# Kernel optimization log

Measured on AMD Instinct MI355X. Metric: run time of the kernel, lower is better.

Reference implementation:

```python
import jax, jax.numpy as jnp
import numpy as np

N = 100000
F_IN = 128
H = 128
E = 1600000
EP = 200000


def _gcn_conv(x, W, b, src, dst, n):
    # GCNConv (PyG default): add self-loops done by caller; symmetric norm; linear + scatter-add.
    xw = x @ W                                        # [n, H]
    deg = jax.ops.segment_sum(jnp.ones(src.shape[0], x.dtype), dst, num_segments=n)
    dinv = jnp.where(deg > 0, jax.lax.rsqrt(deg), 0.0)
    norm = dinv[src] * dinv[dst]                      # [E']
    msg = xw[src] * norm[:, None]                     # [E', H] gather
    out = jax.ops.segment_sum(msg, dst, num_segments=n)  # scatter-add
    return out + b


def setup_inputs() -> dict:
    key = jax.random.key(0)
    k = jax.random.split(key, 9)
    x = jax.random.normal(k[0], (N, F_IN), dtype=jnp.float32)
    edge_index = jax.random.randint(k[1], (2, E), 0, N, dtype=jnp.int64)
    dict_node = jax.random.randint(k[2], (N,), 0, N, dtype=jnp.int64)
    pos_edge_index = jax.random.randint(k[3], (2, EP), 0, N, dtype=jnp.int64)
    neg_edge_index = jax.random.randint(k[4], (2, EP), 0, N, dtype=jnp.int64)
    s1 = 1.0 / np.sqrt(F_IN)
    s2 = 1.0 / np.sqrt(H)
    W1 = jax.random.uniform(k[5], (F_IN, H), jnp.float32, -s1, s1)
    b1 = jnp.zeros((H,), jnp.float32)
    W2 = jax.random.uniform(k[6], (H, H), jnp.float32, -s2, s2)
    b2 = jnp.zeros((H,), jnp.float32)
    return {"x": x, "W1": W1, "b1": b1, "W2": W2, "b2": b2,
            "edge_index": edge_index, "dict_node": dict_node,
            "pos_edge_index": pos_edge_index, "neg_edge_index": neg_edge_index}


def reference(x, W1, b1, W2, b2, edge_index, dict_node, pos_edge_index, neg_edge_index):
    n = x.shape[0]
    # add self-loops once (both convs use the same edge_index)
    loop = jnp.arange(n, dtype=edge_index.dtype)
    src = jnp.concatenate([edge_index[0], loop])
    dst = jnp.concatenate([edge_index[1], loop])
    # encode (dropout p=0.01 is identity in eval mode)
    h = jax.nn.relu(_gcn_conv(x, W1, b1, src, dst, n))
    h = jax.nn.relu(_gcn_conv(h, W2, b2, src, dst, n))
    # global_mean_pool over dict_node segments (size = num_nodes)
    sums = jax.ops.segment_sum(h, dict_node, num_segments=n)
    cnt = jax.ops.segment_sum(jnp.ones((n,), h.dtype), dict_node, num_segments=n)
    z = sums / jnp.maximum(cnt, 1.0)[:, None]
    # decode: per-edge dot products over concatenated pos/neg edges
    ei = jnp.concatenate([pos_edge_index, neg_edge_index], axis=-1)
    logits = jnp.sum(z[ei[0]] * z[ei[1]], axis=-1)
    return logits
```

## Files before the change

kernel.cpp:

```cpp
#include <hip/hip_runtime.h>
#include <hip/hip_fp16.h>

#define HH 128
#define SCAN_T 256
#define SCAN_C 2048
#define PCHUNK 16384


__global__ void hist_k(const int* __restrict__ key, int* __restrict__ hist, int e) {
  int i = blockIdx.x * blockDim.x + threadIdx.x;
  if (i < e) atomicAdd(&hist[key[i]], 1);
}

__global__ __launch_bounds__(SCAN_T) void scan_pass1_k(const int* __restrict__ hist,
                                                       int* __restrict__ bsum, int n) {
  __shared__ int lds[SCAN_T];
  int base = blockIdx.x * SCAN_C + threadIdx.x * 8;
  int s = 0;
  #pragma unroll
  for (int k = 0; k < 8; ++k) { int i = base + k; if (i < n) s += hist[i]; }
  lds[threadIdx.x] = s;
  __syncthreads();
  for (int off = 128; off > 0; off >>= 1) {
    if (threadIdx.x < off) lds[threadIdx.x] += lds[threadIdx.x + off];
    __syncthreads();
  }
  if (threadIdx.x == 0) bsum[blockIdx.x] = lds[0];
}

__global__ __launch_bounds__(SCAN_T) void scan_pass2_k(int* __restrict__ bsum, int nb,
                                                       int* __restrict__ rowptr_n, int total) {
  __shared__ int lds[SCAN_T];
  int v = (threadIdx.x < nb) ? bsum[threadIdx.x] : 0;
  lds[threadIdx.x] = v;
  __syncthreads();
  for (int off = 1; off < SCAN_T; off <<= 1) {
    int t = (threadIdx.x >= off) ? lds[threadIdx.x - off] : 0;
    __syncthreads();
    lds[threadIdx.x] += t;
    __syncthreads();
  }
  if (threadIdx.x < nb) bsum[threadIdx.x] = (threadIdx.x == 0) ? 0 : lds[threadIdx.x - 1];
  if (threadIdx.x == 0) *rowptr_n = total;
}

__global__ __launch_bounds__(SCAN_T) void scan_pass3_k(int* __restrict__ tmp,
                                                       const int* __restrict__ bsum,
                                                       int* __restrict__ rowptr,
                                                       float* __restrict__ dinv, int n) {
  __shared__ int lds[SCAN_T];
  int base = blockIdx.x * SCAN_C + threadIdx.x * 8;
  int v[8]; int s = 0;
  #pragma unroll
  for (int k = 0; k < 8; ++k) { int i = base + k; v[k] = (i < n) ? tmp[i] : 0; s += v[k]; }
  lds[threadIdx.x] = s;
  __syncthreads();
  for (int off = 1; off < SCAN_T; off <<= 1) {
    int t = (threadIdx.x >= off) ? lds[threadIdx.x - off] : 0;
    __syncthreads();
    lds[threadIdx.x] += t;
    __syncthreads();
  }
  int run = bsum[blockIdx.x] + ((threadIdx.x == 0) ? 0 : lds[threadIdx.x - 1]);
  #pragma unroll
  for (int k = 0; k < 8; ++k) {
    int i = base + k;
    if (i < n) {
      rowptr[i] = run;
      tmp[i] = run;
      if (dinv) dinv[i] = rsqrtf((float)v[k] + 1.0f);
      run += v[k];
    }
  }
}

__global__ void build_nodes_k(const int* __restrict__ dict, int* __restrict__ cursor,
                              int* __restrict__ nodelist, int n) {
  int i = blockIdx.x * blockDim.x + threadIdx.x;
  if (i < n) {
    int pos = atomicAdd(&cursor[dict[i]], 1);
    nodelist[pos] = i;
  }
}


__global__ __launch_bounds__(256) void part_count_k(const int* __restrict__ dst, int e,
                                                    int nbkt, int nblk,
                                                    int* __restrict__ gcnt,
                                                    int* __restrict__ blkoff) {
  __shared__ int h[512];
  for (int i = threadIdx.x; i < nbkt; i += 256) h[i] = 0;
  __syncthreads();
  int start = blockIdx.x * PCHUNK;
  int cnt = e - start; if (cnt > PCHUNK) cnt = PCHUNK;
  for (int i = threadIdx.x; i < cnt; i += 256)
    atomicAdd(&h[dst[start + i] >> 8], 1);
  __syncthreads();
  for (int i = threadIdx.x; i < nbkt; i += 256) {
    int c = h[i];
    if (c) blkoff[(size_t)i * nblk + blockIdx.x] = atomicAdd(&gcnt[i], c);
  }
}

__global__ __launch_bounds__(512) void scan_bkt_k(const int* __restrict__ gcnt,
                                                  int* __restrict__ bktbase, int nbkt, int e) {
  __shared__ int sc[512];
  int tid = threadIdx.x;
  int v = (tid < nbkt) ? gcnt[tid] : 0;
  sc[tid] = v;
  __syncthreads();
  for (int off = 1; off < 512; off <<= 1) {
    int t = (tid >= off) ? sc[tid - off] : 0;
    __syncthreads();
    sc[tid] += t;
    __syncthreads();
  }
  if (tid < nbkt) bktbase[tid] = sc[tid] - v;
  if (tid == 0) bktbase[nbkt] = e;
}

__global__ __launch_bounds__(256) void part_scatter_k(const int* __restrict__ src,
                                                      const int* __restrict__ dst, int e,
                                                      int nbkt, int nblk,
                                                      const int* __restrict__ bktbase,
                                                      const int* __restrict__ blkoff,
                                                      int2* __restrict__ part) {
  __shared__ int cur[512];
  for (int i = threadIdx.x; i < nbkt; i += 256)
    cur[i] = bktbase[i] + blkoff[(size_t)i * nblk + blockIdx.x];
  __syncthreads();
  int start = blockIdx.x * PCHUNK;
  int cnt = e - start; if (cnt > PCHUNK) cnt = PCHUNK;
  for (int i = threadIdx.x; i < cnt; i += 256) {
    int d = dst[start + i], s = src[start + i];
    int pos = atomicAdd(&cur[d >> 8], 1);
    part[pos] = make_int2(s, d);
  }
}

__global__ __launch_bounds__(256) void bucket_csr_k(const int2* __restrict__ part,
                                                    const int* __restrict__ bktbase,
                                                    int* __restrict__ rowptr,
                                                    float* __restrict__ dinv,
                                                    int* __restrict__ esrc,
                                                    int n, int e, int nbkt) {
  __shared__ int hist[256];
  __shared__ int sc[256];
  __shared__ int cur[256];
  int tid = threadIdx.x;
  int b = blockIdx.x;
  int dstbase = b << 8;
  int nloc = n - dstbase; if (nloc > 256) nloc = 256;
  int beg = bktbase[b], bend = bktbase[b + 1];

  hist[tid] = 0;
  __syncthreads();
  for (int j = beg + tid; j < bend; j += 256)
    atomicAdd(&hist[part[j].y & 255], 1);
  __syncthreads();
  int v = hist[tid];
  sc[tid] = v;
  __syncthreads();
  for (int off = 1; off < 256; off <<= 1) {
    int t = (tid >= off) ? sc[tid - off] : 0;
    __syncthreads();
    sc[tid] += t;
    __syncthreads();
  }
  int excl = sc[tid] - v;
  if (tid < nloc) {
    rowptr[dstbase + tid] = beg + excl;
    cur[tid] = beg + excl;
    dinv[dstbase + tid] = rsqrtf((float)v + 1.0f);
  }
  __syncthreads();
  for (int j = beg + tid; j < bend; j += 256) {
    int2 p = part[j];
    int pos = atomicAdd(&cur[p.y & 255], 1);
    esrc[pos] = p.x;
  }
  if (b == nbkt - 1 && tid == 0) rowptr[n] = e;
}

template <bool OUT16>
__global__ __launch_bounds__(256) void gemm128_v3(const float* __restrict__ A,
                                                  const float* __restrict__ W,
                                                  const float* __restrict__ dscale,
                                                  void* __restrict__ out, int n) {
  __shared__ float As[64][129];
  const int tid = threadIdx.x;
  const int rbase = blockIdx.x * 64;

  const int vrows = (n - rbase) < 64 ? (n - rbase) : 64;
  const int maxf4 = vrows * 32;
  const float4* Ag = (const float4*)(A + (size_t)rbase * HH);
  #pragma unroll
  for (int j = 0; j < 8; ++j) {
    int f = tid + 256 * j;
    int r = f >> 5, c4 = f & 31;
    float4 v = (f < maxf4) ? Ag[f] : make_float4(0.f, 0.f, 0.f, 0.f);
    As[r][c4 * 4 + 0] = v.x;
    As[r][c4 * 4 + 1] = v.y;
    As[r][c4 * 4 + 2] = v.z;
    As[r][c4 * 4 + 3] = v.w;
  }
  __syncthreads();

  const int r = tid & 63;
  const int q = __builtin_amdgcn_readfirstlane(tid >> 6);
  const float* Asr = &As[r][0];
  const float* Wq = W + q * 32;

  float4 acc[8];
  #pragma unroll
  for (int c = 0; c < 8; ++c) acc[c] = make_float4(0.f, 0.f, 0.f, 0.f);

  #pragma unroll 4
  for (int k = 0; k < HH; ++k) {
    float a = Asr[k];
    const float4* Wr = (const float4*)(Wq + (size_t)k * HH);
    #pragma unroll
    for (int c = 0; c < 8; ++c) {
      float4 w = Wr[c];
      acc[c].x += a * w.x; acc[c].y += a * w.y;
      acc[c].z += a * w.z; acc[c].w += a * w.w;
    }
  }

  int row = rbase + r;
  if (row < n) {
    float s = dscale ? dscale[row] : 1.0f;
    if (OUT16) {
      uint2* o = (uint2*)((__half*)out + (size_t)row * HH) + q * 8;
      #pragma unroll
      for (int c = 0; c < 8; ++c) {
        __half2 h0 = __float22half2_rn(make_float2(acc[c].x * s, acc[c].y * s));
        __half2 h1 = __float22half2_rn(make_float2(acc[c].z * s, acc[c].w * s));
        uint2 u;
        u.x = *reinterpret_cast<unsigned*>(&h0);
        u.y = *reinterpret_cast<unsigned*>(&h1);
        o[c] = u;
      }
    } else {
      float4* o = (float4*)((float*)out + (size_t)row * HH + q * 32);
      #pragma unroll
      for (int c = 0; c < 8; ++c) {
        acc[c].x *= s; acc[c].y *= s; acc[c].z *= s; acc[c].w *= s;
        o[c] = acc[c];
      }
    }
  }
}

__global__ __launch_bounds__(256) void gather16_k(const __half* __restrict__ xw16,
                                                  const int* __restrict__ rowptr,
                                                  const int* __restrict__ esrc,
                                                  const float* __restrict__ dinv,
                                                  const float* __restrict__ bias,
                                                  float* __restrict__ h, int n) {
  int wid = (int)((blockIdx.x * (size_t)blockDim.x + threadIdx.x) >> 6);
  int lane = threadIdx.x & 63;
  if (wid >= n) return;
  int beg = rowptr[wid], end = rowptr[wid + 1];
  int half = lane >> 5, l32 = lane & 31;
  const uint2* base = (const uint2*)xw16 + l32;
  float4 acc = make_float4(0.f, 0.f, 0.f, 0.f);

  for (int j0 = beg; j0 < end; j0 += 64) {
    int myj = j0 + lane;
    int sv = (myj < end) ? esrc[myj] : 0;
    int cnt = end - j0; if (cnt > 64) cnt = 64;
    int k = 0;
    for (; k + 8 <= cnt; k += 8) {
      #pragma unroll
      for (int p = 0; p < 4; ++p) {
        int sa = __builtin_amdgcn_readlane(sv, k + 2 * p);
        int sb = __builtin_amdgcn_readlane(sv, k + 2 * p + 1);
        unsigned off = (unsigned)(half ? sb : sa) << 5;
        uint2 u = base[off];
        float2 f0 = __half22float2(*reinterpret_cast<__half2*>(&u.x));
        float2 f1 = __half22float2(*reinterpret_cast<__half2*>(&u.y));
        acc.x += f0.x; acc.y += f0.y; acc.z += f1.x; acc.w += f1.y;
      }
    }
    for (; k + 2 <= cnt; k += 2) {
      int sa = __builtin_amdgcn_readlane(sv, k);
      int sb = __builtin_amdgcn_readlane(sv, k + 1);
      unsigned off = (unsigned)(half ? sb : sa) << 5;
      uint2 u = base[off];
      float2 f0 = __half22float2(*reinterpret_cast<__half2*>(&u.x));
      float2 f1 = __half22float2(*reinterpret_cast<__half2*>(&u.y));
      acc.x += f0.x; acc.y += f0.y; acc.z += f1.x; acc.w += f1.y;
    }
    if (k < cnt) {
      int sa = __builtin_amdgcn_readlane(sv, k);
      if (half == 0) {
        uint2 u = base[(unsigned)sa << 5];
        float2 f0 = __half22float2(*reinterpret_cast<__half2*>(&u.x));
        float2 f1 = __half22float2(*reinterpret_cast<__half2*>(&u.y));
        acc.x += f0.x; acc.y += f0.y; acc.z += f1.x; acc.w += f1.y;
      }
    }
  }
  acc.x += __shfl_xor(acc.x, 32);
  acc.y += __shfl_xor(acc.y, 32);
  acc.z += __shfl_xor(acc.z, 32);
  acc.w += __shfl_xor(acc.w, 32);
  if (half == 0) {
    uint2 u = base[(unsigned)wid << 5];
    float2 s0 = __half22float2(*reinterpret_cast<__half2*>(&u.x));
    float2 s1 = __half22float2(*reinterpret_cast<__half2*>(&u.y));
    float di = dinv[wid];
    float4 bb = ((const float4*)bias)[l32];
    float4 o;
    o.x = fmaxf(bb.x + di * (acc.x + s0.x), 0.f);
    o.y = fmaxf(bb.y + di * (acc.y + s0.y), 0.f);
    o.z = fmaxf(bb.z + di * (acc.z + s1.x), 0.f);
    o.w = fmaxf(bb.w + di * (acc.w + s1.y), 0.f);
    ((float4*)h)[((size_t)wid << 5) + l32] = o;
  }
}

__global__ __launch_bounds__(256) void decode_fused2_k(const float* __restrict__ h2,
                                                       const int* __restrict__ rowptr,
                                                       const int* __restrict__ nodelist,
                                                       const int* __restrict__ pos,
                                                       const int* __restrict__ neg,
                                                       float* __restrict__ out, int ep) {
  int wv = (int)((blockIdx.x * (size_t)blockDim.x + threadIdx.x) >> 6);
  int lane = threadIdx.x & 63;
  int qq = lane >> 4, l16 = lane & 15;
  int e0 = wv * 2;
  if (e0 >= 2 * ep) return;
  int edge = e0 + (qq >> 1);
  int side = qq & 1;
  bool live = edge < 2 * ep;
  int eL = live ? edge : 2 * ep - 1;
  int node;
  if (eL < ep) node = side ? pos[ep + eL] : pos[eL];
  else { int t = eL - ep; node = side ? neg[ep + t] : neg[t]; }

  int beg = rowptr[node], end = rowptr[node + 1];
  const float4* h4 = (const float4*)h2;
  float4 a0 = make_float4(0.f, 0.f, 0.f, 0.f);
  float4 a1 = make_float4(0.f, 0.f, 0.f, 0.f);

  int m = (beg < end) ? nodelist[beg] : 0;
  for (int j = beg; j < end; ++j) {
    int mn = (j + 1 < end) ? nodelist[j + 1] : 0;
    const float4* r = h4 + ((size_t)m << 5);
    float4 v0 = r[l16], v1 = r[l16 + 16];
    a0.x += v0.x; a0.y += v0.y; a0.z += v0.z; a0.w += v0.w;
    a1.x += v1.x; a1.y += v1.y; a1.z += v1.z; a1.w += v1.w;
    m = mn;
  }
  float inv = 1.0f / fmaxf((float)(end - beg), 1.0f);
  a0.x *= inv; a0.y *= inv; a0.z *= inv; a0.w *= inv;
  a1.x *= inv; a1.y *= inv; a1.z *= inv; a1.w *= inv;

  float4 b0, b1;
  b0.x = __shfl_xor(a0.x, 16); b0.y = __shfl_xor(a0.y, 16);
  b0.z = __shfl_xor(a0.z, 16); b0.w = __shfl_xor(a0.w, 16);
  b1.x = __shfl_xor(a1.x, 16); b1.y = __shfl_xor(a1.y, 16);
  b1.z = __shfl_xor(a1.z, 16); b1.w = __shfl_xor(a1.w, 16);
  float p = a0.x * b0.x + a0.y * b0.y + a0.z * b0.z + a0.w * b0.w
          + a1.x * b1.x + a1.y * b1.y + a1.z * b1.z + a1.w * b1.w;
  #pragma unroll
  for (int off = 8; off > 0; off >>= 1) p += __shfl_xor(p, off);
  if (live && side == 0 && l16 == 0) out[edge] = p;
}

__global__ void fill_deg_k(float* __restrict__ deg, int n) {
  int i = blockIdx.x * blockDim.x + threadIdx.x;
  if (i < n) deg[i] = 1.0f;
}
__global__ void accum_deg_k(const int* __restrict__ dst, float* __restrict__ deg, int e) {
  int i = blockIdx.x * blockDim.x + threadIdx.x;
  if (i < e) atomicAdd(&deg[dst[i]], 1.0f);
}
__global__ void dinv_k(float* __restrict__ deg, int n) {
  int i = blockIdx.x * blockDim.x + threadIdx.x;
  if (i < n) deg[i] = rsqrtf(deg[i]);
}
__global__ void init_h_k(const float* __restrict__ xw, const float* __restrict__ bias,
                         const float* __restrict__ dinv, float* __restrict__ h, int n) {
  int gid = blockIdx.x * blockDim.x + threadIdx.x;
  int node = gid >> 5, c4 = gid & 31;
  if (node >= n) return;
  float di = dinv[node];
  float nm = di * di;
  float4 v = ((const float4*)(xw + (size_t)node * HH))[c4];
  float4 b = ((const float4*)bias)[c4];
  ((float4*)(h + (size_t)node * HH))[c4] =
      make_float4(b.x + nm * v.x, b.y + nm * v.y, b.z + nm * v.z, b.w + nm * v.w);
}
__global__ void scatter_k(const float* __restrict__ xw, float* __restrict__ h,
                          const float* __restrict__ dinv, const int* __restrict__ src,
                          const int* __restrict__ dst, int e) {
  int gid = blockIdx.x * blockDim.x + threadIdx.x;
  int edge = gid >> 5, lane = gid & 31;
  if (edge >= e) return;
  int s = src[edge], d = dst[edge];
  float norm = dinv[s] * dinv[d];
  float4 v = ((const float4*)(xw + (size_t)s * HH))[lane];
  float* o = h + (size_t)d * HH + lane * 4;
  atomicAdd(o + 0, norm * v.x);
  atomicAdd(o + 1, norm * v.y);
  atomicAdd(o + 2, norm * v.z);
  atomicAdd(o + 3, norm * v.w);
}
__global__ void relu_k(float4* __restrict__ h, int n4) {
  int i = blockIdx.x * blockDim.x + threadIdx.x;
  if (i < n4) {
    float4 v = h[i];
    v.x = fmaxf(v.x, 0.f); v.y = fmaxf(v.y, 0.f);
    v.z = fmaxf(v.z, 0.f); v.w = fmaxf(v.w, 0.f);
    h[i] = v;
  }
}
__global__ void pool_accum_k(const float* __restrict__ h, const int* __restrict__ dict,
                             float* __restrict__ z, float* __restrict__ cnt, int n) {
  int gid = blockIdx.x * blockDim.x + threadIdx.x;
  int node = gid >> 5, lane = gid & 31;
  if (node >= n) return;
  int d = dict[node];
  float4 v = ((const float4*)(h + (size_t)node * HH))[lane];
  float* o = z + (size_t)d * HH + lane * 4;
  atomicAdd(o + 0, v.x); atomicAdd(o + 1, v.y);
  atomicAdd(o + 2, v.z); atomicAdd(o + 3, v.w);
  if (lane == 0) atomicAdd(&cnt[d], 1.0f);
}
__global__ void pool_div_k(float* __restrict__ z, const float* __restrict__ cnt, int n) {
  int gid = blockIdx.x * blockDim.x + threadIdx.x;
  int node = gid >> 5, lane = gid & 31;
  if (node >= n) return;
  float inv = 1.0f / fmaxf(cnt[node], 1.0f);
  float4* p = (float4*)(z + (size_t)node * HH) + lane;
  float4 v = *p;
  v.x *= inv; v.y *= inv; v.z *= inv; v.w *= inv;
  *p = v;
}
__global__ void decode_k(const float* __restrict__ z, const int* __restrict__ pos,
                         const int* __restrict__ neg, float* __restrict__ out, int ep) {
  int gid = blockIdx.x * blockDim.x + threadIdx.x;
  int edge = gid >> 5, lane = gid & 31;
  if (edge >= 2 * ep) return;
  int a, b;
  if (edge < ep) { a = pos[edge];      b = pos[ep + edge]; }
  else           { a = neg[edge - ep]; b = neg[edge]; }
  const float4* za = (const float4*)(z + (size_t)a * HH);
  const float4* zb = (const float4*)(z + (size_t)b * HH);
  float4 va = za[lane], vb = zb[lane];
  float dot = va.x * vb.x + va.y * vb.y + va.z * vb.z + va.w * vb.w;
  #pragma unroll
  for (int off = 16; off > 0; off >>= 1) dot += __shfl_xor(dot, off);
  if (lane == 0) out[edge] = dot;
}

extern "C" void kernel_launch(void* const* d_in, const int* in_sizes, int n_in,
                              void* d_out, int out_size, void* d_ws, size_t ws_size,
                              hipStream_t stream) {
  const float* x  = (const float*)d_in[0];
  const float* W1 = (const float*)d_in[1];
  const float* b1 = (const float*)d_in[2];
  const float* W2 = (const float*)d_in[3];
  const float* b2 = (const float*)d_in[4];
  const int* ei   = (const int*)d_in[5];
  const int* dict = (const int*)d_in[6];
  const int* pe   = (const int*)d_in[7];
  const int* ne   = (const int*)d_in[8];

  const int n  = in_sizes[0] / HH;
  const int e  = in_sizes[5] / 2;
  const int ep = in_sizes[7] / 2;
  const int* src = ei;
  const int* dst = ei + e;

  const size_t nf = (size_t)n * HH;
  const int nbkt = (n + 255) >> 8;
  const int nblk = (e + PCHUNK - 1) / PCHUNK;

  float*  p0     = (float*)d_ws;
  float*  bufF   = p0;
  __half* xw16   = (__half*)(p0 + nf);
  float*  dinv   = p0 + nf + nf / 2;
  int*    rowptr = (int*)(dinv + n);
  int*    tmp    = rowptr + (n + 1);
  int*    esrc   = tmp + n;
  int*    bsum   = esrc + e;
  int*    gcnt   = bsum + 256;
  int*    bktbase = gcnt + nbkt;
  size_t need = (nf + nf / 2 + n) * sizeof(float) +
                (size_t)(3 * n + 1 + e + 256 + 2 * nbkt + 1) * sizeof(int);

  int2* part   = (int2*)bufF;
  int*  blkoff = (int*)xw16;

  const int nb    = (n + 255) / 256;
  const int nb32  = (int)(((size_t)n * 32 + 255) / 256);
  const int nb64  = (int)(((size_t)n * 64 + 255) / 256);
  const int gemb  = (n + 63) / 64;
  const int NBS   = (n + SCAN_C - 1) / SCAN_C;
  const int deb2  = (int)(((size_t)ep * 64 + 255) / 256);

  bool fast = (ws_size >= need) && (nbkt <= 512) &&
              ((size_t)nbkt * nblk * 2 <= nf) && ((size_t)e * 2 <= nf);

  if (fast) {
    hipMemsetAsync(gcnt, 0, (size_t)nbkt * sizeof(int), stream);
    part_count_k<<<nblk, 256, 0, stream>>>(dst, e, nbkt, nblk, gcnt, blkoff);
    scan_bkt_k<<<1, 512, 0, stream>>>(gcnt, bktbase, nbkt, e);
    part_scatter_k<<<nblk, 256, 0, stream>>>(src, dst, e, nbkt, nblk, bktbase, blkoff, part);
    bucket_csr_k<<<nbkt, 256, 0, stream>>>(part, bktbase, rowptr, dinv, esrc, n, e, nbkt);

    gemm128_v3<true><<<gemb, 256, 0, stream>>>(x, W1, dinv, xw16, n);
    gather16_k<<<nb64, 256, 0, stream>>>(xw16, rowptr, esrc, dinv, b1, bufF, n);
    gemm128_v3<true><<<gemb, 256, 0, stream>>>(bufF, W2, dinv, xw16, n);
    gather16_k<<<nb64, 256, 0, stream>>>(xw16, rowptr, esrc, dinv, b2, bufF, n);

    hipMemsetAsync(tmp, 0, (size_t)n * sizeof(int), stream);
    hist_k<<<nb, 256, 0, stream>>>(dict, tmp, n);
    scan_pass1_k<<<NBS, SCAN_T, 0, stream>>>(tmp, bsum, n);
    scan_pass2_k<<<1, SCAN_T, 0, stream>>>(bsum, NBS, rowptr + n, n);
    scan_pass3_k<<<NBS, SCAN_T, 0, stream>>>(tmp, bsum, rowptr, nullptr, n);
    build_nodes_k<<<nb, 256, 0, stream>>>(dict, tmp, esrc, n);

    decode_fused2_k<<<deb2, 256, 0, stream>>>(bufF, rowptr, esrc, pe, ne, (float*)d_out, ep);
  } else {
    float* bufA  = (float*)d_ws;
    float* bufB  = bufA + nf;
    float* dinv2 = bufB + nf;
    float* cnt   = dinv2 + n;
    fill_deg_k<<<nb, 256, 0, stream>>>(dinv2, n);
    accum_deg_k<<<(e + 255) / 256, 256, 0, stream>>>(dst, dinv2, e);
    dinv_k<<<nb, 256, 0, stream>>>(dinv2, n);

    gemm128_v3<false><<<gemb, 256, 0, stream>>>(x, W1, nullptr, bufA, n);
    init_h_k<<<nb32, 256, 0, stream>>>(bufA, b1, dinv2, bufB, n);
    scatter_k<<<(int)(((size_t)e * 32 + 255) / 256), 256, 0, stream>>>(bufA, bufB, dinv2, src, dst, e);
    relu_k<<<nb32, 256, 0, stream>>>((float4*)bufB, n * 32);

    gemm128_v3<false><<<gemb, 256, 0, stream>>>(bufB, W2, nullptr, bufA, n);
    init_h_k<<<nb32, 256, 0, stream>>>(bufA, b2, dinv2, bufB, n);
    scatter_k<<<(int)(((size_t)e * 32 + 255) / 256), 256, 0, stream>>>(bufA, bufB, dinv2, src, dst, e);
    relu_k<<<nb32, 256, 0, stream>>>((float4*)bufB, n * 32);

    hipMemsetAsync(bufA, 0, nf * sizeof(float), stream);
    hipMemsetAsync(cnt, 0, (size_t)n * sizeof(float), stream);
    pool_accum_k<<<nb32, 256, 0, stream>>>(bufB, dict, bufA, cnt, n);
    pool_div_k<<<nb32, 256, 0, stream>>>(bufA, cnt, n);
    decode_k<<<(int)(((size_t)2 * ep * 32 + 255) / 256), 256, 0, stream>>>(
        bufA, pe, ne, (float*)d_out, ep);
  }
}
```

Baseline: 413.6 us.

## Reuse bucket partition for pool CSR, split GEMM LDS tile, unroll decode gather

Builds the pooling node lists with the same two-level bucket partition used for the edge CSR, replacing the global-atomic histogram, three-pass scan and atomic node scatter. The GEMM now stages A in two 64-column halves, which halves its shared memory and may allow more resident blocks, at the cost of an extra barrier. The decode pooling loop processes two nodes per iteration with separate accumulators to expose more memory-level parallelism. Together these are meant to cut kernel count, contended atomics and latency stalls.

New measurement: 406.9 us. No clear change (-1.6%).

```diff
diff --git a/kernel.cpp b/kernel.cpp
--- a/kernel.cpp
+++ b/kernel.cpp
@@ -2,89 +2,10 @@
 #include <hip/hip_fp16.h>
 
 #define HH 128
-#define SCAN_T 256
-#define SCAN_C 2048
 #define PCHUNK 16384
 
 
-__global__ void hist_k(const int* __restrict__ key, int* __restrict__ hist, int e) {
-  int i = blockIdx.x * blockDim.x + threadIdx.x;
-  if (i < e) atomicAdd(&hist[key[i]], 1);
-}
-
-__global__ __launch_bounds__(SCAN_T) void scan_pass1_k(const int* __restrict__ hist,
-                                                       int* __restrict__ bsum, int n) {
-  __shared__ int lds[SCAN_T];
-  int base = blockIdx.x * SCAN_C + threadIdx.x * 8;
-  int s = 0;
-  #pragma unroll
-  for (int k = 0; k < 8; ++k) { int i = base + k; if (i < n) s += hist[i]; }
-  lds[threadIdx.x] = s;
-  __syncthreads();
-  for (int off = 128; off > 0; off >>= 1) {
-    if (threadIdx.x < off) lds[threadIdx.x] += lds[threadIdx.x + off];
-    __syncthreads();
-  }
-  if (threadIdx.x == 0) bsum[blockIdx.x] = lds[0];
-}
-
-__global__ __launch_bounds__(SCAN_T) void scan_pass2_k(int* __restrict__ bsum, int nb,
-                                                       int* __restrict__ rowptr_n, int total) {
-  __shared__ int lds[SCAN_T];
-  int v = (threadIdx.x < nb) ? bsum[threadIdx.x] : 0;
-  lds[threadIdx.x] = v;
-  __syncthreads();
-  for (int off = 1; off < SCAN_T; off <<= 1) {
-    int t = (threadIdx.x >= off) ? lds[threadIdx.x - off] : 0;
-    __syncthreads();
-    lds[threadIdx.x] += t;
-    __syncthreads();
-  }
-  if (threadIdx.x < nb) bsum[threadIdx.x] = (threadIdx.x == 0) ? 0 : lds[threadIdx.x - 1];
-  if (threadIdx.x == 0) *rowptr_n = total;
-}
-
-__global__ __launch_bounds__(SCAN_T) void scan_pass3_k(int* __restrict__ tmp,
-                                                       const int* __restrict__ bsum,
-                                                       int* __restrict__ rowptr,
-                                                       float* __restrict__ dinv, int n) {
-  __shared__ int lds[SCAN_T];
-  int base = blockIdx.x * SCAN_C + threadIdx.x * 8;
-  int v[8]; int s = 0;
-  #pragma unroll
-  for (int k = 0; k < 8; ++k) { int i = base + k; v[k] = (i < n) ? tmp[i] : 0; s += v[k]; }
-  lds[threadIdx.x] = s;
-  __syncthreads();
-  for (int off = 1; off < SCAN_T; off <<= 1) {
-    int t = (threadIdx.x >= off) ? lds[threadIdx.x - off] : 0;
-    __syncthreads();
-    lds[threadIdx.x] += t;
-    __syncthreads();
-  }
-  int run = bsum[blockIdx.x] + ((threadIdx.x == 0) ? 0 : lds[threadIdx.x - 1]);
-  #pragma unroll
-  for (int k = 0; k < 8; ++k) {
-    int i = base + k;
-    if (i < n) {
-      rowptr[i] = run;
-      tmp[i] = run;
-      if (dinv) dinv[i] = rsqrtf((float)v[k] + 1.0f);
-      run += v[k];
-    }
-  }
-}
-
-__global__ void build_nodes_k(const int* __restrict__ dict, int* __restrict__ cursor,
-                              int* __restrict__ nodelist, int n) {
-  int i = blockIdx.x * blockDim.x + threadIdx.x;
-  if (i < n) {
-    int pos = atomicAdd(&cursor[dict[i]], 1);
-    nodelist[pos] = i;
-  }
-}
-
-
-__global__ __launch_bounds__(256) void part_count_k(const int* __restrict__ dst, int e,
+__global__ __launch_bounds__(256) void part_count_k(const int* __restrict__ key, int e,
                                                     int nbkt, int nblk,
                                                     int* __restrict__ gcnt,
                                                     int* __restrict__ blkoff) {
@@ -94,7 +15,7 @@
   int start = blockIdx.x * PCHUNK;
   int cnt = e - start; if (cnt > PCHUNK) cnt = PCHUNK;
   for (int i = threadIdx.x; i < cnt; i += 256)
-    atomicAdd(&h[dst[start + i] >> 8], 1);
+    atomicAdd(&h[key[start + i] >> 8], 1);
   __syncthreads();
   for (int i = threadIdx.x; i < nbkt; i += 256) {
     int c = h[i];
@@ -120,7 +41,7 @@
 }
 
 __global__ __launch_bounds__(256) void part_scatter_k(const int* __restrict__ src,
-                                                      const int* __restrict__ dst, int e,
+                                                      const int* __restrict__ key, int e,
                                                       int nbkt, int nblk,
                                                       const int* __restrict__ bktbase,
                                                       const int* __restrict__ blkoff,
@@ -132,9 +53,27 @@
   int start = blockIdx.x * PCHUNK;
   int cnt = e - start; if (cnt > PCHUNK) cnt = PCHUNK;
   for (int i = threadIdx.x; i < cnt; i += 256) {
-    int d = dst[start + i], s = src[start + i];
+    int d = key[start + i], s = src[start + i];
     int pos = atomicAdd(&cur[d >> 8], 1);
     part[pos] = make_int2(s, d);
+  }
+}
+
+__global__ __launch_bounds__(256) void part_scatter_idx_k(const int* __restrict__ key, int e,
+                                                          int nbkt, int nblk,
+                                                          const int* __restrict__ bktbase,
+                                                          const int* __restrict__ blkoff,
+                                                          int2* __restrict__ part) {
+  __shared__ int cur[512];
+  for (int i = threadIdx.x; i < nbkt; i += 256)
+    cur[i] = bktbase[i] + blkoff[(size_t)i * nblk + blockIdx.x];
+  __syncthreads();
+  int start = blockIdx.x * PCHUNK;
+  int cnt = e - start; if (cnt > PCHUNK) cnt = PCHUNK;
+  for (int i = threadIdx.x; i < cnt; i += 256) {
+    int d = key[start + i];
+    int pos = atomicAdd(&cur[d >> 8], 1);
+    part[pos] = make_int2(start + i, d);
   }
 }
 
@@ -171,7 +110,7 @@
   if (tid < nloc) {
     rowptr[dstbase + tid] = beg + excl;
     cur[tid] = beg + excl;
-    dinv[dstbase + tid] = rsqrtf((float)v + 1.0f);
+    if (dinv) dinv[dstbase + tid] = rsqrtf((float)v + 1.0f);
   }
   __syncthreads();
   for (int j = beg + tid; j < bend; j += 256) {
@@ -183,47 +122,50 @@
 }
 
 template <bool OUT16>
-__global__ __launch_bounds__(256) void gemm128_v3(const float* __restrict__ A,
+__global__ __launch_bounds__(256) void gemm128_v4(const float* __restrict__ A,
                                                   const float* __restrict__ W,
                                                   const float* __restrict__ dscale,
                                                   void* __restrict__ out, int n) {
-  __shared__ float As[64][129];
+  __shared__ float As[64][65];
   const int tid = threadIdx.x;
   const int rbase = blockIdx.x * 64;
-
   const int vrows = (n - rbase) < 64 ? (n - rbase) : 64;
-  const int maxf4 = vrows * 32;
-  const float4* Ag = (const float4*)(A + (size_t)rbase * HH);
-  #pragma unroll
-  for (int j = 0; j < 8; ++j) {
-    int f = tid + 256 * j;
-    int r = f >> 5, c4 = f & 31;
-    float4 v = (f < maxf4) ? Ag[f] : make_float4(0.f, 0.f, 0.f, 0.f);
-    As[r][c4 * 4 + 0] = v.x;
-    As[r][c4 * 4 + 1] = v.y;
-    As[r][c4 * 4 + 2] = v.z;
-    As[r][c4 * 4 + 3] = v.w;
-  }
-  __syncthreads();
 
   const int r = tid & 63;
   const int q = __builtin_amdgcn_readfirstlane(tid >> 6);
-  const float* Asr = &As[r][0];
   const float* Wq = W + q * 32;
 
   float4 acc[8];
   #pragma unroll
   for (int c = 0; c < 8; ++c) acc[c] = make_float4(0.f, 0.f, 0.f, 0.f);
 
-  #pragma unroll 4
-  for (int k = 0; k < HH; ++k) {
-    float a = Asr[k];
-    const float4* Wr = (const float4*)(Wq + (size_t)k * HH);
+  #pragma unroll
+  for (int ph = 0; ph < 2; ++ph) {
+    if (ph) __syncthreads();
     #pragma unroll
-    for (int c = 0; c < 8; ++c) {
-      float4 w = Wr[c];
-      acc[c].x += a * w.x; acc[c].y += a * w.y;
-      acc[c].z += a * w.z; acc[c].w += a * w.w;
+    for (int j = 0; j < 4; ++j) {
+      int f = tid + 256 * j;
+      int rr = f >> 4, c4 = f & 15;
+      float4 v = (rr < vrows)
+          ? ((const float4*)(A + (size_t)(rbase + rr) * HH + ph * 64))[c4]
+          : make_float4(0.f, 0.f, 0.f, 0.f);
+      As[rr][c4 * 4 + 0] = v.x;
+      As[rr][c4 * 4 + 1] = v.y;
+      As[rr][c4 * 4 + 2] = v.z;
+      As[rr][c4 * 4 + 3] = v.w;
+    }
+    __syncthreads();
+
+    #pragma unroll 4
+    for (int kk = 0; kk < 64; ++kk) {
+      float a = As[r][kk];
+      const float4* Wr = (const float4*)(Wq + (size_t)(ph * 64 + kk) * HH);
+      #pragma unroll
+      for (int c = 0; c < 8; ++c) {
+        float4 w = Wr[c];
+        acc[c].x += a * w.x; acc[c].y += a * w.y;
+        acc[c].z += a * w.z; acc[c].w += a * w.w;
+      }
     }
   }
 
@@ -321,7 +263,7 @@
   }
 }
 
-__global__ __launch_bounds__(256) void decode_fused2_k(const float* __restrict__ h2,
+__global__ __launch_bounds__(256) void decode_fused3_k(const float* __restrict__ h2,
                                                        const int* __restrict__ rowptr,
                                                        const int* __restrict__ nodelist,
                                                        const int* __restrict__ pos,
@@ -344,16 +286,27 @@
   const float4* h4 = (const float4*)h2;
   float4 a0 = make_float4(0.f, 0.f, 0.f, 0.f);
   float4 a1 = make_float4(0.f, 0.f, 0.f, 0.f);
-
-  int m = (beg < end) ? nodelist[beg] : 0;
-  for (int j = beg; j < end; ++j) {
-    int mn = (j + 1 < end) ? nodelist[j + 1] : 0;
-    const float4* r = h4 + ((size_t)m << 5);
-    float4 v0 = r[l16], v1 = r[l16 + 16];
-    a0.x += v0.x; a0.y += v0.y; a0.z += v0.z; a0.w += v0.w;
-    a1.x += v1.x; a1.y += v1.y; a1.z += v1.z; a1.w += v1.w;
-    m = mn;
-  }
+  float4 c0 = make_float4(0.f, 0.f, 0.f, 0.f);
+  float4 c1 = make_float4(0.f, 0.f, 0.f, 0.f);
+
+  for (int j = beg; j < end; j += 2) {
+    bool two = (j + 1) < end;
+    int m0 = nodelist[j];
+    int m1 = two ? nodelist[j + 1] : m0;
+    const float4* r0 = h4 + ((size_t)m0 << 5);
+    const float4* r1 = h4 + ((size_t)m1 << 5);
+    float4 u0 = r0[l16], u1 = r0[l16 + 16];
+    float4 v0 = r1[l16], v1 = r1[l16 + 16];
+    a0.x += u0.x; a0.y += u0.y; a0.z += u0.z; a0.w += u0.w;
+    a1.x += u1.x; a1.y += u1.y; a1.z += u1.z; a1.w += u1.w;
+    if (two) {
+      c0.x += v0.x; c0.y += v0.y; c0.z += v0.z; c0.w += v0.w;
+      c1.x += v1.x; c1.y += v1.y; c1.z += v1.z; c1.w += v1.w;
+    }
+  }
+  a0.x += c0.x; a0.y += c0.y; a0.z += c0.z; a0.w += c0.w;
+  a1.x += c1.x; a1.y += c1.y; a1.z += c1.z; a1.w += c1.w;
+
   float inv = 1.0f / fmaxf((float)(end - beg), 1.0f);
   a0.x *= inv; a0.y *= inv; a0.z *= inv; a0.w *= inv;
   a1.x *= inv; a1.y *= inv; a1.z *= inv; a1.w *= inv;
@@ -477,8 +430,9 @@
   const int* dst = ei + e;
 
   const size_t nf = (size_t)n * HH;
-  const int nbkt = (n + 255) >> 8;
-  const int nblk = (e + PCHUNK - 1) / PCHUNK;
+  const int nbkt  = (n + 255) >> 8;
+  const int nblkE = (e + PCHUNK - 1) / PCHUNK;
+  const int nblkN = (n + PCHUNK - 1) / PCHUNK;
 
   float*  p0     = (float*)d_ws;
   float*  bufF   = p0;
@@ -493,39 +447,39 @@
   size_t need = (nf + nf / 2 + n) * sizeof(float) +
                 (size_t)(3 * n + 1 + e + 256 + 2 * nbkt + 1) * sizeof(int);
 
-  int2* part   = (int2*)bufF;
-  int*  blkoff = (int*)xw16;
+  int2* partE   = (int2*)bufF;
+  int*  blkoffE = (int*)xw16;
+  int2* partN   = (int2*)xw16;
+  int*  blkoffN = (int*)(partN + n);
 
   const int nb    = (n + 255) / 256;
   const int nb32  = (int)(((size_t)n * 32 + 255) / 256);
   const int nb64  = (int)(((size_t)n * 64 + 255) / 256);
   const int gemb  = (n + 63) / 64;
-  const int NBS   = (n + SCAN_C - 1) / SCAN_C;
   const int deb2  = (int)(((size_t)ep * 64 + 255) / 256);
 
   bool fast = (ws_size >= need) && (nbkt <= 512) &&
-              ((size_t)nbkt * nblk * 2 <= nf) && ((size_t)e * 2 <= nf);
+              ((size_t)nbkt * nblkE * 2 <= nf) && ((size_t)e * 2 <= nf);
 
   if (fast) {
     hipMemsetAsync(gcnt, 0, (size_t)nbkt * sizeof(int), stream);
-    part_count_k<<<nblk, 256, 0, stream>>>(dst, e, nbkt, nblk, gcnt, blkoff);
+    part_count_k<<<nblkE, 256, 0, stream>>>(dst, e, nbkt, nblkE, gcnt, blkoffE);
     scan_bkt_k<<<1, 512, 0, stream>>>(gcnt, bktbase, nbkt, e);
-    part_scatter_k<<<nblk, 256, 0, stream>>>(src, dst, e, nbkt, nblk, bktbase, blkoff, part);
-    bucket_csr_k<<<nbkt, 256, 0, stream>>>(part, bktbase, rowptr, dinv, esrc, n, e, nbkt);
-
-    gemm128_v3<true><<<gemb, 256, 0, stream>>>(x, W1, dinv, xw16, n);
+    part_scatter_k<<<nblkE, 256, 0, stream>>>(src, dst, e, nbkt, nblkE, bktbase, blkoffE, partE);
+    bucket_csr_k<<<nbkt, 256, 0, stream>>>(partE, bktbase, rowptr, dinv, esrc, n, e, nbkt);
+
+    gemm128_v4<true><<<gemb, 256, 0, stream>>>(x, W1, dinv, xw16, n);
     gather16_k<<<nb64, 256, 0, stream>>>(xw16, rowptr, esrc, dinv, b1, bufF, n);
-    gemm128_v3<true><<<gemb, 256, 0, stream>>>(bufF, W2, dinv, xw16, n);
+    gemm128_v4<true><<<gemb, 256, 0, stream>>>(bufF, W2, dinv, xw16, n);
     gather16_k<<<nb64, 256, 0, stream>>>(xw16, rowptr, esrc, dinv, b2, bufF, n);
 
-    hipMemsetAsync(tmp, 0, (size_t)n * sizeof(int), stream);
-    hist_k<<<nb, 256, 0, stream>>>(dict, tmp, n);
-    scan_pass1_k<<<NBS, SCAN_T, 0, stream>>>(tmp, bsum, n);
-    scan_pass2_k<<<1, SCAN_T, 0, stream>>>(bsum, NBS, rowptr + n, n);
-    scan_pass3_k<<<NBS, SCAN_T, 0, stream>>>(tmp, bsum, rowptr, nullptr, n);
-    build_nodes_k<<<nb, 256, 0, stream>>>(dict, tmp, esrc, n);
-
-    decode_fused2_k<<<deb2, 256, 0, stream>>>(bufF, rowptr, esrc, pe, ne, (float*)d_out, ep);
+    hipMemsetAsync(gcnt, 0, (size_t)nbkt * sizeof(int), stream);
+    part_count_k<<<nblkN, 256, 0, stream>>>(dict, n, nbkt, nblkN, gcnt, blkoffN);
+    scan_bkt_k<<<1, 512, 0, stream>>>(gcnt, bktbase, nbkt, n);
+    part_scatter_idx_k<<<nblkN, 256, 0, stream>>>(dict, n, nbkt, nblkN, bktbase, blkoffN, partN);
+    bucket_csr_k<<<nbkt, 256, 0, stream>>>(partN, bktbase, rowptr, nullptr, esrc, n, n, nbkt);
+
+    decode_fused3_k<<<deb2, 256, 0, stream>>>(bufF, rowptr, esrc, pe, ne, (float*)d_out, ep);
   } else {
     float* bufA  = (float*)d_ws;
     float* bufB  = bufA + nf;
@@ -535,12 +489,12 @@
     accum_deg_k<<<(e + 255) / 256, 256, 0, stream>>>(dst, dinv2, e);
     dinv_k<<<nb, 256, 0, stream>>>(dinv2, n);
 
-    gemm128_v3<false><<<gemb, 256, 0, stream>>>(x, W1, nullptr, bufA, n);
+    gemm128_v4<false><<<gemb, 256, 0, stream>>>(x, W1, nullptr, bufA, n);
     init_h_k<<<nb32, 256, 0, stream>>>(bufA, b1, dinv2, bufB, n);
     scatter_k<<<(int)(((size_t)e * 32 + 255) / 256), 256, 0, stream>>>(bufA, bufB, dinv2, src, dst, e);
     relu_k<<<nb32, 256, 0, stream>>>((float4*)bufB, n * 32);
 
-    gemm128_v3<false><<<gemb, 256, 0, stream>>>(bufB, W2, nullptr, bufA, n);
+    gemm128_v4<false><<<gemb, 256, 0, stream>>>(bufB, W2, nullptr, bufA, n);
     init_h_k<<<nb32, 256, 0, stream>>>(bufA, b2, dinv2, bufB, n);
     scatter_k<<<(int)(((size_t)e * 32 + 255) / 256), 256, 0, stream>>>(bufA, bufB, dinv2, src, dst, e);
     relu_k<<<nb32, 256, 0, stream>>>((float4*)bufB, n * 32);
```
